# Kernel optimization log

Hardware: AMD Instinct MI355X
Metric: run time of the kernel (lower is better)

## Reference

```python
import jax, jax.numpy as jnp
import numpy as np

B, S, D = 4, 8192, 1024

def log_g(x):
    # log of g(x): log(x + 0.5) for x >= 0, log(sigmoid(x)) = -softplus(-x) otherwise
    return jnp.where(x >= 0, jnp.log(jax.nn.relu(x) + 0.5), -jax.nn.softplus(-x))

def setup_inputs() -> dict:
    key = jax.random.key(0)
    k1, k2 = jax.random.split(key)
    x = jax.random.normal(k1, (B, S, D), dtype=jnp.float32)
    # Linear(dim, 3*dim, bias=False); stored as [dim, 3*dim] so y = x @ W
    W = jax.random.normal(k2, (D, 3 * D), dtype=jnp.float32) * (1.0 / np.sqrt(D))
    return {"x": x, "W": W}

def reference(x, W):
    # x: [B, S, D], W: [D, 3D]
    hW = jnp.einsum('bsd,de->bse', x, W)  # [B, S, 3D]
    hidden, f_gate, i_gate = jnp.split(hW, 3, axis=-1)

    # log-space normalized gates:
    # diff = softplus(-f) - softplus(-i); log_f' = -softplus(diff); log_i' = -softplus(-diff)
    diff = jax.nn.softplus(-f_gate) - jax.nn.softplus(-i_gate)
    log_f = -jax.nn.softplus(diff)
    log_i = -jax.nn.softplus(-diff)
    log_values = log_i + log_g(hidden)

    # Heinsen associative scan in log space (float32 internally)
    a_star = jnp.cumsum(log_f.astype(jnp.float32), axis=1)
    log_h0_plus_b_star = jax.lax.cumlogsumexp(log_values.astype(jnp.float32) - a_star, axis=1)
    log_h = a_star + log_h0_plus_b_star
    out = jnp.exp(log_h).astype(x.dtype)  # [B, S, D]
    return out
```

## Files before the change

kernel.cpp:

```cpp
#include <hip/hip_runtime.h>
#include <hip/hip_bf16.h>
#include <cstdint>
#include <cstddef>


#define BB 4
#define SS 8192
#define DD 1024
#define MM 32768
#define KK 1024
#define NN 3072
#define CHUNKS 256
#define CLEN 32
#define NCH 4096

typedef __bf16 bf16;
typedef __bf16 bf16x2 __attribute__((ext_vector_type(2)));
typedef __bf16 bf16x4 __attribute__((ext_vector_type(4)));
typedef __bf16 bf16x8 __attribute__((ext_vector_type(8)));
typedef float f32x4 __attribute__((ext_vector_type(4)));

__device__ __forceinline__ void gload16(const bf16* g, bf16* l) {
  __builtin_amdgcn_global_load_lds(
      (const __attribute__((address_space(1))) unsigned int*)(const void*)g,
      (__attribute__((address_space(3))) unsigned int*)(void*)l,
      16, 0, 0);
}

__device__ __forceinline__ float sp(float x) {
  return fmaxf(x, 0.f) + __logf(1.f + __expf(-fabsf(x)));
}
__device__ __forceinline__ void gates(float h, float f, float i,
                                      float& lf, float& lv) {
  float d = sp(-f) - sp(-i);
  float spd = sp(d);
  lf = -spd;
  float li = d - spd;
  float lg = (h >= 0.f) ? __logf(h + 0.5f) : -sp(-h);
  lv = li + lg;
}
__device__ __forceinline__ float laddexp(float a, float b) {
  float m = fmaxf(a, b);
  return m + __logf(1.f + __expf(fminf(a, b) - m));
}
__device__ __forceinline__ void comb(float& A, float& V, float Ac, float Vc) {
  V = laddexp(V + Ac, Vc);
  A += Ac;
}

__global__ __launch_bounds__(256) void k_cvt_x(const float4* __restrict__ x,
                                               bf16x4* __restrict__ xb) {
  int i = blockIdx.x * 256 + threadIdx.x;
  float4 v = x[i];
  bf16x4 o;
  o[0] = (bf16)v.x; o[1] = (bf16)v.y; o[2] = (bf16)v.z; o[3] = (bf16)v.w;
  xb[i] = o;
}

__global__ __launch_bounds__(256) void k_cvt_wt(const float* __restrict__ W,
                                                bf16* __restrict__ Wt) {
  __shared__ float tile[32][33];
  int n0 = blockIdx.x * 32, k0 = blockIdx.y * 32;
  int tx = threadIdx.x, ty = threadIdx.y;
#pragma unroll
  for (int i = 0; i < 32; i += 8)
    tile[ty + i][tx] = W[(size_t)(k0 + ty + i) * NN + n0 + tx];
  __syncthreads();
#pragma unroll
  for (int i = 0; i < 32; i += 8)
    Wt[(size_t)(n0 + ty + i) * KK + k0 + tx] = (bf16)tile[tx][ty + i];
}

__global__ __launch_bounds__(256) void k_gemm(const bf16* __restrict__ A,
                                              const bf16* __restrict__ Bt,
                                              bf16* __restrict__ C) {
  __shared__ bf16 smem[64 * 132];
  bf16* As = smem;
  bf16* Bs = smem + 4096;
  const int tid = threadIdx.x;
  const int nBase = blockIdx.x * 128;
  const int mBase = blockIdx.y * 128;
  const int lane = tid & 63;
  const int w = tid >> 6;
  const int wm = (w >> 1) * 64, wn = (w & 1) * 64;
  const int col16 = lane & 15;
  const int kq = (lane >> 4) * 8;
  const int r0 = tid >> 2;
  const int cc = (tid & 3) * 8;
  const bf16* ga0 = A + (size_t)(mBase + r0) * KK + cc;
  const bf16* ga1 = A + (size_t)(mBase + 64 + r0) * KK + cc;
  const bf16* gb0 = Bt + (size_t)(nBase + r0) * KK + cc;
  const bf16* gb1 = Bt + (size_t)(nBase + 64 + r0) * KK + cc;
  bf16* la = As + tid * 8;
  bf16* lb = Bs + tid * 8;

  f32x4 acc[4][4];
#pragma unroll
  for (int mi = 0; mi < 4; ++mi)
#pragma unroll
    for (int ni = 0; ni < 4; ++ni)
      acc[mi][ni] = (f32x4){0.f, 0.f, 0.f, 0.f};

  for (int k0 = 0; k0 < KK; k0 += 32) {
    gload16(ga0 + k0, la);
    gload16(ga1 + k0, la + 2048);
    gload16(gb0 + k0, lb);
    gload16(gb1 + k0, lb + 2048);
    __syncthreads();
    bf16x8 afr[4], bfr[4];
#pragma unroll
    for (int mi = 0; mi < 4; ++mi)
      afr[mi] = *(const bf16x8*)(As + (wm + mi * 16 + col16) * 32 + kq);
#pragma unroll
    for (int ni = 0; ni < 4; ++ni)
      bfr[ni] = *(const bf16x8*)(Bs + (wn + ni * 16 + col16) * 32 + kq);
#pragma unroll
    for (int mi = 0; mi < 4; ++mi)
#pragma unroll
      for (int ni = 0; ni < 4; ++ni)
        acc[mi][ni] = __builtin_amdgcn_mfma_f32_16x16x32_bf16(
            afr[mi], bfr[ni], acc[mi][ni], 0, 0, 0);
    __syncthreads();
  }

  const int rowq = (lane >> 4) * 4;
#pragma unroll
  for (int ph = 0; ph < 2; ++ph) {
    if (wm == ph * 64) {
#pragma unroll
      for (int mi = 0; mi < 4; ++mi)
#pragma unroll
        for (int ni = 0; ni < 4; ++ni)
#pragma unroll
          for (int r = 0; r < 4; ++r)
            smem[(mi * 16 + rowq + r) * 132 + wn + ni * 16 + col16] =
                (bf16)acc[mi][ni][r];
    }
    __syncthreads();
#pragma unroll
    for (int pass = 0; pass < 4; ++pass) {
      int row = pass * 16 + (tid >> 4);
      int col = (tid & 15) * 8;
      bf16x8 v = *(const bf16x8*)(smem + row * 132 + col);
      *(bf16x8*)(C + (size_t)(mBase + ph * 64 + row) * NN + nBase + col) = v;
    }
    __syncthreads();
  }
}

__global__ __launch_bounds__(256, 6) void k_scan1(const bf16* __restrict__ hW,
                                                  float2* __restrict__ agg) {
  const int d0 = (blockIdx.x * 256 + threadIdx.x) * 2;
  const int b = blockIdx.y, c = blockIdx.z;
  const bf16* p = hW + (size_t)(b * SS + c * CLEN) * NN + d0;
  float A0 = 0.f, V0 = -1e30f, A1 = 0.f, V1 = -1e30f;
  bf16x2 hh = *(const bf16x2*)(p);
  bf16x2 ff = *(const bf16x2*)(p + DD);
  bf16x2 ii = *(const bf16x2*)(p + 2 * DD);
#pragma unroll 4
  for (int j = 0; j < CLEN - 1; ++j) {
    p += NN;
    bf16x2 hn = *(const bf16x2*)(p);
    bf16x2 fn = *(const bf16x2*)(p + DD);
    bf16x2 in2 = *(const bf16x2*)(p + 2 * DD);
    float lf, lv;
    gates((float)hh[0], (float)ff[0], (float)ii[0], lf, lv);
    A0 += lf; V0 = laddexp(V0 + lf, lv);
    gates((float)hh[1], (float)ff[1], (float)ii[1], lf, lv);
    A1 += lf; V1 = laddexp(V1 + lf, lv);
    hh = hn; ff = fn; ii = in2;
  }
  float lf, lv;
  gates((float)hh[0], (float)ff[0], (float)ii[0], lf, lv);
  A0 += lf; V0 = laddexp(V0 + lf, lv);
  gates((float)hh[1], (float)ff[1], (float)ii[1], lf, lv);
  A1 += lf; V1 = laddexp(V1 + lf, lv);
  const size_t ch = (size_t)b * DD + d0;
  agg[ch * CHUNKS + c] = make_float2(A0, V0);
  agg[(ch + 1) * CHUNKS + c] = make_float2(A1, V1);
}

__global__ __launch_bounds__(256) void k_scan2(const float2* __restrict__ agg,
                                               float2* __restrict__ pre) {
  const int ch = blockIdx.x * 4 + (threadIdx.x >> 6);
  const int lane = threadIdx.x & 63;
  const float4* src = (const float4*)(agg + (size_t)ch * CHUNKS);
  float4 v0 = src[lane * 2];
  float4 v1 = src[lane * 2 + 1];
  float A = v0.x, V = v0.y;
  comb(A, V, v0.z, v0.w);
  comb(A, V, v1.x, v1.y);
  comb(A, V, v1.z, v1.w);
#pragma unroll
  for (int off = 1; off < 64; off <<= 1) {
    float Ao = __shfl_up(A, off);
    float Vo = __shfl_up(V, off);
    if (lane >= off) {
      V = laddexp(Vo + A, V);
      A = Ao + A;
    }
  }
  float exA = __shfl_up(A, 1);
  float exV = __shfl_up(V, 1);
  if (lane == 0) { exA = 0.f; exV = -1e30f; }
  float4 o0, o1;
  o0.x = exA; o0.y = exV;
  comb(exA, exV, v0.x, v0.y);
  o0.z = exA; o0.w = exV;
  comb(exA, exV, v0.z, v0.w);
  o1.x = exA; o1.y = exV;
  comb(exA, exV, v1.x, v1.y);
  o1.z = exA; o1.w = exV;
  float4* dst = (float4*)(pre + (size_t)ch * CHUNKS);
  dst[lane * 2] = o0;
  dst[lane * 2 + 1] = o1;
}

__global__ __launch_bounds__(256, 6) void k_scan3(const bf16* __restrict__ hW,
                                                  const float2* __restrict__ pre,
                                                  float* __restrict__ out) {
  const int d0 = (blockIdx.x * 256 + threadIdx.x) * 2;
  const int b = blockIdx.y, c = blockIdx.z;
  const bf16* p = hW + (size_t)(b * SS + c * CLEN) * NN + d0;
  float* o = out + (size_t)(b * SS + c * CLEN) * DD + d0;
  const size_t ch = (size_t)b * DD + d0;
  float V0 = pre[ch * CHUNKS + c].y;
  float V1 = pre[(ch + 1) * CHUNKS + c].y;
  bf16x2 hh = *(const bf16x2*)(p);
  bf16x2 ff = *(const bf16x2*)(p + DD);
  bf16x2 ii = *(const bf16x2*)(p + 2 * DD);
#pragma unroll 4
  for (int j = 0; j < CLEN - 1; ++j) {
    p += NN;
    bf16x2 hn = *(const bf16x2*)(p);
    bf16x2 fn = *(const bf16x2*)(p + DD);
    bf16x2 in2 = *(const bf16x2*)(p + 2 * DD);
    float lf, lv;
    gates((float)hh[0], (float)ff[0], (float)ii[0], lf, lv);
    V0 = laddexp(V0 + lf, lv);
    gates((float)hh[1], (float)ff[1], (float)ii[1], lf, lv);
    V1 = laddexp(V1 + lf, lv);
    *(float2*)o = make_float2(__expf(V0), __expf(V1));
    o += DD;
    hh = hn; ff = fn; ii = in2;
  }
  float lf, lv;
  gates((float)hh[0], (float)ff[0], (float)ii[0], lf, lv);
  V0 = laddexp(V0 + lf, lv);
  gates((float)hh[1], (float)ff[1], (float)ii[1], lf, lv);
  V1 = laddexp(V1 + lf, lv);
  *(float2*)o = make_float2(__expf(V0), __expf(V1));
}

extern "C" void kernel_launch(void* const* d_in, const int* in_sizes, int n_in,
                              void* d_out, int out_size, void* d_ws,
                              size_t ws_size, hipStream_t stream) {
  const float* x = (const float*)d_in[0];
  const float* W = (const float*)d_in[1];
  float* out = (float*)d_out;
  char* ws = (char*)d_ws;

  const size_t wtB = (size_t)NN * KK * 2;
  const size_t xbB = (size_t)MM * KK * 2;
  const size_t aggB = (size_t)CHUNKS * NCH * sizeof(float2);
  bf16* Wt = (bf16*)ws;
  bf16* xb = (bf16*)(ws + wtB);
  bf16* hW = (bf16*)(ws + wtB + xbB);
  float2* agg = (float2*)(ws + wtB);
  float2* pre = (float2*)(ws + wtB + aggB);

  k_cvt_wt<<<dim3(NN / 32, KK / 32), dim3(32, 8), 0, stream>>>(W, Wt);
  k_cvt_x<<<dim3(MM * KK / 4 / 256), dim3(256), 0, stream>>>((const float4*)x,
                                                             (bf16x4*)xb);
  k_gemm<<<dim3(NN / 128, MM / 128), 256, 0, stream>>>(xb, Wt, hW);
  k_scan1<<<dim3(DD / 512, BB, CHUNKS), 256, 0, stream>>>(hW, agg);
  k_scan2<<<dim3(NCH / 4), 256, 0, stream>>>(agg, pre);
  k_scan3<<<dim3(DD / 512, BB, CHUNKS), 256, 0, stream>>>(hW, pre, out);
}
```

Baseline: 638.5 us.

## Rewrite GEMM as 256x256 tiled, double-buffered, swizzled-LDS 8-wave kernel

Replaces the 128x128 single-buffered bf16 GEMM with a 256x256 tile per 512-thread block, with K-step 64 and double-buffered LDS loads issued via global_load_lds. LDS columns are XOR-swizzled to avoid bank conflicts, block IDs are remapped for L2 locality, and MFMA quadrants are interleaved with the next stage's loads under raised wave priority. The aim is higher arithmetic intensity and latency hiding for the dominant GEMM. The cost is 128KB of LDS per block, which limits occupancy, and more complex barrier-based scheduling.

```diff
diff --git a/kernel.cpp b/kernel.cpp
--- a/kernel.cpp
+++ b/kernel.cpp
@@ -13,6 +13,7 @@
 #define CHUNKS 256
 #define CLEN 32
 #define NCH 4096
+#define NT 16
 
 typedef __bf16 bf16;
 typedef __bf16 bf16x2 __attribute__((ext_vector_type(2)));
@@ -71,81 +72,164 @@
     Wt[(size_t)(n0 + ty + i) * KK + k0 + tx] = (bf16)tile[tx][ty + i];
 }
 
-__global__ __launch_bounds__(256) void k_gemm(const bf16* __restrict__ A,
-                                              const bf16* __restrict__ Bt,
-                                              bf16* __restrict__ C) {
-  __shared__ bf16 smem[64 * 132];
-  bf16* As = smem;
-  bf16* Bs = smem + 4096;
+__global__ __launch_bounds__(512, 2) void k_gemm(const bf16* __restrict__ A,
+                                                 const bf16* __restrict__ Bt,
+                                                 bf16* __restrict__ C) {
+  __shared__ __align__(16) bf16 sm[65536];
   const int tid = threadIdx.x;
-  const int nBase = blockIdx.x * 128;
-  const int mBase = blockIdx.y * 128;
   const int lane = tid & 63;
   const int w = tid >> 6;
-  const int wm = (w >> 1) * 64, wn = (w & 1) * 64;
-  const int col16 = lane & 15;
-  const int kq = (lane >> 4) * 8;
-  const int r0 = tid >> 2;
-  const int cc = (tid & 3) * 8;
-  const bf16* ga0 = A + (size_t)(mBase + r0) * KK + cc;
-  const bf16* ga1 = A + (size_t)(mBase + 64 + r0) * KK + cc;
-  const bf16* gb0 = Bt + (size_t)(nBase + r0) * KK + cc;
-  const bf16* gb1 = Bt + (size_t)(nBase + 64 + r0) * KK + cc;
-  bf16* la = As + tid * 8;
-  bf16* lb = Bs + tid * 8;
-
-  f32x4 acc[4][4];
-#pragma unroll
-  for (int mi = 0; mi < 4; ++mi)
-#pragma unroll
-    for (int ni = 0; ni < 4; ++ni)
-      acc[mi][ni] = (f32x4){0.f, 0.f, 0.f, 0.f};
-
-  for (int k0 = 0; k0 < KK; k0 += 32) {
-    gload16(ga0 + k0, la);
-    gload16(ga1 + k0, la + 2048);
-    gload16(gb0 + k0, lb);
-    gload16(gb1 + k0, lb + 2048);
-    __syncthreads();
-    bf16x8 afr[4], bfr[4];
-#pragma unroll
-    for (int mi = 0; mi < 4; ++mi)
-      afr[mi] = *(const bf16x8*)(As + (wm + mi * 16 + col16) * 32 + kq);
-#pragma unroll
-    for (int ni = 0; ni < 4; ++ni)
-      bfr[ni] = *(const bf16x8*)(Bs + (wn + ni * 16 + col16) * 32 + kq);
-#pragma unroll
-    for (int mi = 0; mi < 4; ++mi)
-#pragma unroll
-      for (int ni = 0; ni < 4; ++ni)
-        acc[mi][ni] = __builtin_amdgcn_mfma_f32_16x16x32_bf16(
-            afr[mi], bfr[ni], acc[mi][ni], 0, 0, 0);
-    __syncthreads();
-  }
-
-  const int rowq = (lane >> 4) * 4;
-#pragma unroll
-  for (int ph = 0; ph < 2; ++ph) {
-    if (wm == ph * 64) {
+  const int wm = w >> 2;
+  const int wn = w & 3;
+  const int c16 = lane & 15;
+  const int l4 = lane >> 4;
+
+  int bid = blockIdx.x;
+  int swz = (bid & 7) * 192 + (bid >> 3);
+  int mT = swz / 12;
+  int nT = swz - mT * 12;
+  const int mBase = mT * 256, nBase = nT * 256;
+
+  const int sr = tid >> 3;
+  const int scol = ((tid & 7) ^ (sr & 7)) * 8;
+  const bf16* gA = A + (size_t)(mBase + sr) * KK + scol;
+  const bf16* gB = Bt + (size_t)(nBase + sr) * KK + scol;
+  const int ld = tid * 8;
+
+  const int sw8 = c16 & 7;
+  const int sx0 = (l4 ^ sw8) * 8;
+  const int sx1 = ((l4 + 4) ^ sw8) * 8;
+  const int aRow = (wm * 64 + c16) * 64;
+  const int bRow = (wn * 32 + c16) * 64;
+
+  f32x4 acc[2][2][4][2];
+#pragma unroll
+  for (int a = 0; a < 2; ++a)
+#pragma unroll
+    for (int b2 = 0; b2 < 2; ++b2)
+#pragma unroll
+      for (int m = 0; m < 4; ++m)
+#pragma unroll
+        for (int n = 0; n < 2; ++n)
+          acc[a][b2][m][n] = (f32x4){0.f, 0.f, 0.f, 0.f};
+
+#define STGA(h, L, bo, ko) \
+  gload16(gA + (h) * 131072 + (L) * 65536 + (ko), \
+          sm + (bo) + (h) * 8192 + (L) * 4096 + ld)
+#define STGB(h, L, bo, ko) \
+  gload16(gB + (h) * 131072 + (L) * 65536 + (ko), \
+          sm + (bo) + 16384 + (h) * 8192 + (L) * 4096 + ld)
+#define LDA(qm)                                                         \
+  _Pragma("unroll") for (int mi = 0; mi < 4; ++mi) {                    \
+    const bf16* p_ = sm + buf + (qm) * 8192 + aRow + mi * 1024;         \
+    afr[mi][0] = *(const bf16x8*)(p_ + sx0);                            \
+    afr[mi][1] = *(const bf16x8*)(p_ + sx1);                            \
+  }
+#define LDB(qn)                                                         \
+  _Pragma("unroll") for (int ni = 0; ni < 2; ++ni) {                    \
+    const bf16* p_ = sm + buf + 16384 + (qn) * 8192 + bRow + ni * 1024; \
+    bfr[ni][0] = *(const bf16x8*)(p_ + sx0);                            \
+    bfr[ni][1] = *(const bf16x8*)(p_ + sx1);                            \
+  }
+#define MFMAQ(qm, qn)                                                     \
+  __builtin_amdgcn_s_setprio(1);                                          \
+  _Pragma("unroll") for (int mi = 0; mi < 4; ++mi)                        \
+  _Pragma("unroll") for (int ni = 0; ni < 2; ++ni) {                      \
+    acc[qm][qn][mi][ni] = __builtin_amdgcn_mfma_f32_16x16x32_bf16(        \
+        afr[mi][0], bfr[ni][0], acc[qm][qn][mi][ni], 0, 0, 0);            \
+    acc[qm][qn][mi][ni] = __builtin_amdgcn_mfma_f32_16x16x32_bf16(        \
+        afr[mi][1], bfr[ni][1], acc[qm][qn][mi][ni], 0, 0, 0);            \
+  }                                                                       \
+  __builtin_amdgcn_s_setprio(0);
+#define BAR asm volatile("s_barrier" ::: "memory")
+#define VMC(n) asm volatile("s_waitcnt vmcnt(" #n ")" ::: "memory")
+
+  STGA(0, 0, 0, 0); STGA(0, 1, 0, 0); STGB(0, 0, 0, 0); STGB(0, 1, 0, 0);
+  STGA(1, 0, 0, 0); STGA(1, 1, 0, 0); STGB(1, 0, 0, 0); STGB(1, 1, 0, 0);
+  VMC(4);
+  BAR;
+
+  bf16x8 afr[4][2], bfr[2][2];
+
+  for (int t = 0; t < NT - 1; ++t) {
+    const int buf = (t & 1) << 15;
+    const int nb = buf ^ 32768;
+    const int ko = (t + 1) * 64;
+    LDA(0); LDB(0);
+    STGA(0, 0, nb, ko); STGA(0, 1, nb, ko);
+    STGB(0, 0, nb, ko); STGB(0, 1, nb, ko);
+    VMC(4);
+    BAR;
+    MFMAQ(0, 0);
+    BAR;
+    LDA(1);
+    STGA(1, 0, nb, ko); STGA(1, 1, nb, ko);
+    BAR;
+    MFMAQ(1, 0);
+    BAR;
+    LDB(1);
+    STGB(1, 0, nb, ko); STGB(1, 1, nb, ko);
+    BAR;
+    MFMAQ(1, 1);
+    BAR;
+    LDA(0);
+    VMC(4);
+    BAR;
+    MFMAQ(0, 1);
+    BAR;
+  }
+  {
+    const int buf = 32768;
+    LDA(0); LDB(0);
+    VMC(0);
+    BAR;
+    MFMAQ(0, 0);
+    BAR;
+    LDA(1);
+    BAR;
+    MFMAQ(1, 0);
+    BAR;
+    LDB(1);
+    BAR;
+    MFMAQ(1, 1);
+    BAR;
+    LDA(0);
+    BAR;
+    MFMAQ(0, 1);
+  }
+
+  __syncthreads();
+  const int rq = l4 * 4;
+#pragma unroll
+  for (int qm = 0; qm < 2; ++qm)
+#pragma unroll
+    for (int qn = 0; qn < 2; ++qn)
 #pragma unroll
       for (int mi = 0; mi < 4; ++mi)
 #pragma unroll
-        for (int ni = 0; ni < 4; ++ni)
-#pragma unroll
-          for (int r = 0; r < 4; ++r)
-            smem[(mi * 16 + rowq + r) * 132 + wn + ni * 16 + col16] =
-                (bf16)acc[mi][ni][r];
-    }
-    __syncthreads();
-#pragma unroll
-    for (int pass = 0; pass < 4; ++pass) {
-      int row = pass * 16 + (tid >> 4);
-      int col = (tid & 15) * 8;
-      bf16x8 v = *(const bf16x8*)(smem + row * 132 + col);
-      *(bf16x8*)(C + (size_t)(mBase + ph * 64 + row) * NN + nBase + col) = v;
-    }
-    __syncthreads();
-  }
+        for (int ni = 0; ni < 2; ++ni)
+#pragma unroll
+          for (int r = 0; r < 4; ++r) {
+            int row = qm * 128 + wm * 64 + mi * 16 + rq + r;
+            int col = (qn * 128 + wn * 32 + ni * 16 + c16) ^ ((row & 7) << 3);
+            sm[row * 256 + col] = (bf16)acc[qm][qn][mi][ni][r];
+          }
+  __syncthreads();
+#pragma unroll
+  for (int p = 0; p < 16; ++p) {
+    int row = p * 16 + (tid >> 5);
+    int colL = (tid & 31) * 8;
+    int col = colL ^ ((row & 7) << 3);
+    bf16x8 v = *(const bf16x8*)(sm + row * 256 + col);
+    *(bf16x8*)(C + (size_t)(mBase + row) * NN + nBase + colL) = v;
+  }
+#undef STGA
+#undef STGB
+#undef LDA
+#undef LDB
+#undef MFMAQ
+#undef BAR
+#undef VMC
 }
 
 __global__ __launch_bounds__(256, 6) void k_scan1(const bf16* __restrict__ hW,
@@ -272,7 +356,7 @@
   k_cvt_wt<<<dim3(NN / 32, KK / 32), dim3(32, 8), 0, stream>>>(W, Wt);
   k_cvt_x<<<dim3(MM * KK / 4 / 256), dim3(256), 0, stream>>>((const float4*)x,
                                                              (bf16x4*)xb);
-  k_gemm<<<dim3(NN / 128, MM / 128), 256, 0, stream>>>(xb, Wt, hW);
+  k_gemm<<<dim3((NN / 256) * (MM / 256)), dim3(512), 0, stream>>>(xb, Wt, hW);
   k_scan1<<<dim3(DD / 512, BB, CHUNKS), 256, 0, stream>>>(hW, agg);
   k_scan2<<<dim3(NCH / 4), 256, 0, stream>>>(agg, pre);
   k_scan3<<<dim3(DD / 512, BB, CHUNKS), 256, 0, stream>>>(hW, pre, out);
```

Measured after the change: 624.4 us. 1.02x faster.
